# Kernel tuning notes

Measured on AMD Instinct MI355X. Metric: run time of the kernel, lower is better.

## Reference

```python
import jax, jax.numpy as jnp
import numpy as np

STEPS = 8  # number of scaling-and-squaring steps


def _identity_grid(D, H, W, dtype):
    # (D, H, W, 3) voxel-coordinate identity transformation
    z = jnp.arange(D, dtype=dtype)
    y = jnp.arange(H, dtype=dtype)
    x = jnp.arange(W, dtype=dtype)
    return jnp.stack(jnp.meshgrid(z, y, x, indexing='ij'), axis=-1)


def _pull_wrap(v, phi):
    """Trilinear sampling of field v at voxel coords phi with circular ('dft') bound.

    v:   (B, D, H, W, 3) vector field (values)
    phi: (B, D, H, W, 3) sampling coordinates in voxel space (z, y, x order)
    """
    B, D, H, W, C = v.shape
    f = jnp.floor(phi)
    w1 = phi - f          # weight of the +1 corner
    w0 = 1.0 - w1
    i0 = f.astype(jnp.int32)
    dims = jnp.array([D, H, W], dtype=jnp.int32)
    i0 = jnp.mod(i0, dims)          # wrap (dft) boundary
    i1 = jnp.mod(i0 + 1, dims)
    zs, ys, xs = (i0[..., 0], i1[..., 0]), (i0[..., 1], i1[..., 1]), (i0[..., 2], i1[..., 2])
    wzs, wys, wxs = (w0[..., 0], w1[..., 0]), (w0[..., 1], w1[..., 1]), (w0[..., 2], w1[..., 2])
    vflat = v.reshape(B, D * H * W, C)
    out = jnp.zeros_like(v)
    for a in range(2):
        for b in range(2):
            for c in range(2):
                lin = (zs[a] * H + ys[b]) * W + xs[c]              # (B, D, H, W)
                vals = jnp.take_along_axis(vflat, lin.reshape(B, -1, 1), axis=1)
                vals = vals.reshape(B, D, H, W, C)
                out = out + (wzs[a] * wys[b] * wxs[c])[..., None] * vals
    return out


def setup_inputs() -> dict:
    key = jax.random.key(0)
    velocity = jax.random.normal(key, (2, 128, 128, 128, 3), dtype=jnp.float32)
    return {"velocity": velocity}


def reference(velocity):
    # Scaling and squaring: v <- v/2^K; repeat K times: v <- v + v o (id + v)
    B, D, H, W, C = velocity.shape
    grid = _identity_grid(D, H, W, velocity.dtype)[None]  # (1, D, H, W, 3)
    v = velocity / (2.0 ** STEPS)
    for _ in range(STEPS):
        v = v + _pull_wrap(v, grid + v)
    # displacement=False -> return transformation field id + displacement
    return grid + v
```

## Files before the change

### kernel.cpp

```cpp
#include <hip/hip_runtime.h>
#include <hip/hip_fp16.h>


#define DHW   (128 * 128 * 128)
#define NVOX  (2 * DHW)
#define RW    129

#if defined(__has_builtin)
#  if __has_builtin(__builtin_amdgcn_global_load_lds)
#    define HAVE_ASYNC 1
#  endif
#endif
#ifndef HAVE_ASYNC
#  define HAVE_ASYNC 0
#endif

__device__ __forceinline__ __half2 bc_h2(unsigned u) {
    return *reinterpret_cast<__half2*>(&u);
}

__device__ __forceinline__ void acc_cell(uint2 c, float w,
                                         float& az, float& ay, float& ax) {
    __half2 c0 = bc_h2(c.x), c1 = bc_h2(c.y);
    az = fmaf(w, __low2float(c0),  az);
    ay = fmaf(w, __high2float(c0), ay);
    ax = fmaf(w, __low2float(c1),  ax);
}

template <int H, int BX, int BZ, bool PAD_OUT>
__global__ __launch_bounds__(512) void sq_sten_dma(
    const uint2* __restrict__ fin, uint2* __restrict__ fout)
{
    constexpr int LBX = (BX == 64) ? 6 : 5;
    constexpr int NB = 4;
    constexpr int TX = BX + 2 * H, TY = 8 + 2 * H, TZ = BZ + 2 * H;
    constexpr int TS = TX * TY * TZ;
    constexpr int DWS = TS * 2;
    constexpr int NP  = (DWS + 511) / 512;
    constexpr int VPT = (BX * BZ) / 64;
    constexpr int NXB = 128 / BX, LNX = 7 - LBX;
    static_assert(2 * TS * 8 <= 64 * 1024, "dbuf exceeds 64KB static LDS");
    static_assert(VPT == 4 || VPT == 2, "vmcnt literal needs 4 or 2");
    __shared__ uint2 bufA[TS];
    __shared__ uint2 bufB[TS];

    int t = (int)threadIdx.x;
    int b = (int)blockIdx.x;
    int X = (b & (NXB - 1)) << LBX;
    int b2 = b >> LNX;
    int Y = (b2 & 15) << 3;
    int b3 = b2 >> 4;
    int Z0 = (b3 & 7) * (BZ * NB);
    int batch = b3 >> 3;
    int bb21 = batch << 21;

    unsigned sxy[NP];
    unsigned szzp[(NP + 3) / 4];
#pragma unroll
    for (int q = 0; q < (NP + 3) / 4; ++q) szzp[q] = 0;
#pragma unroll
    for (int p = 0; p < NP; ++p) {
        int idx = t + p * 512;
        if (idx < DWS) {
            int cell = idx >> 1, half = idx & 1;
            int xx = cell % TX;
            int rem = cell / TX;
            int yy = rem % TY, zz = rem / TY;
            int gx = (X - H + xx) & 127;
            int gy = (Y - H + yy) & 127;
            sxy[p] = (unsigned)((((gy << 7) | gx) << 1) | half);
            szzp[p >> 2] |= (unsigned)zz << ((p & 3) * 8);
        } else {
            sxy[p] = 0;
        }
    }

    const unsigned* fdw = (const unsigned*)fin;

#if HAVE_ASYNC
#define ASYNC_DW(lptr, gptr)                                            \
    __builtin_amdgcn_global_load_lds(                                   \
        (const __attribute__((address_space(1))) unsigned*)(gptr),      \
        (__attribute__((address_space(3))) unsigned*)(lptr), 4, 0, 0)
#else
#define ASYNC_DW(lptr, gptr)  (*(lptr) = *(gptr))
#endif

#define STAGE(ZB, BUF)                                                  \
    { unsigned* ldw = (unsigned*)(BUF);                                 \
      _Pragma("unroll")                                                 \
      for (int p = 0; p < NP; ++p) {                                    \
          int idx = t + p * 512;                                        \
          if (idx < DWS) {                                              \
              int zz = (int)((szzp[p >> 2] >> ((p & 3) * 8)) & 255u);   \
              int gz = ((ZB) - H + zz) & 127;                           \
              ASYNC_DW(ldw + idx,                                       \
                       fdw + (bb21 << 1) + (gz << 15) + (int)sxy[p]);   \
          }                                                             \
      }                                                                 \
      __builtin_amdgcn_sched_barrier(0); }

    int lx = t & (BX - 1);
    int ly = (t >> LBX) & 7;
    int lz0 = (t >> (LBX + 3)) * VPT;

#define COMPUTE(TILE, Z)                                                \
    { _Pragma("unroll")                                                 \
      for (int v = 0; v < VPT; ++v) {                                   \
          int lz = lz0 + v;                                             \
          int cidx = ((lz + H) * TY + (ly + H)) * TX + (lx + H);        \
          uint2 c = (TILE)[cidx];                                       \
          __half2 c0 = bc_h2(c.x), c1 = bc_h2(c.y);                     \
          float vz = __low2float(c0), vy = __high2float(c0);            \
          float vx = __low2float(c1);                                   \
          float pz = (float)((Z) + lz) + vz;                            \
          float py = (float)(Y + ly) + vy;                              \
          float px = (float)(X + lx) + vx;                              \
          float fz = floorf(pz), fy = floorf(py), fx = floorf(px);      \
          float wz1 = pz - fz, wy1 = py - fy, wx1 = px - fx;            \
          float wz0 = 1.0f - wz1, wy0 = 1.0f - wy1, wx0 = 1.0f - wx1;   \
          int izl = (int)fz - (Z) + H;                                  \
          int iyl = (int)fy - Y + H;                                    \
          int ixl = (int)fx - X + H;                                    \
          float wzy00 = wz0 * wy0, wzy01 = wz0 * wy1;                   \
          float wzy10 = wz1 * wy0, wzy11 = wz1 * wy1;                   \
          float az = 0.0f, ay = 0.0f, ax = 0.0f;                        \
          int i00 = (izl * TY + iyl) * TX + ixl;                        \
          int i01 = i00 + TX;                                           \
          int i10 = i00 + TY * TX;                                      \
          int i11 = i10 + TX;                                           \
          acc_cell((TILE)[i00],     wzy00 * wx0, az, ay, ax);           \
          acc_cell((TILE)[i00 + 1], wzy00 * wx1, az, ay, ax);           \
          acc_cell((TILE)[i01],     wzy01 * wx0, az, ay, ax);           \
          acc_cell((TILE)[i01 + 1], wzy01 * wx1, az, ay, ax);           \
          acc_cell((TILE)[i10],     wzy10 * wx0, az, ay, ax);           \
          acc_cell((TILE)[i10 + 1], wzy10 * wx1, az, ay, ax);           \
          acc_cell((TILE)[i11],     wzy11 * wx0, az, ay, ax);           \
          acc_cell((TILE)[i11 + 1], wzy11 * wx1, az, ay, ax);           \
          __half2 p0 = __floats2half2_rn(vz + az, vy + ay);             \
          __half2 p1 = __floats2half2_rn(vx + ax, 0.0f);                \
          uint2 sd;                                                     \
          sd.x = *reinterpret_cast<unsigned*>(&p0);                     \
          sd.y = *reinterpret_cast<unsigned*>(&p1);                     \
          int z_ = (Z) + lz, y_ = Y + ly, x_ = X + lx;                  \
          if (PAD_OUT) {                                                \
              int rS = (batch << 14) + (z_ << 7) + y_;                  \
              int pidx = (rS << 7) + rS + x_;                           \
              fout[pidx] = sd;                                          \
              if (x_ == 0) fout[pidx + 128] = sd;                       \
          } else {                                                      \
              fout[bb21 | (z_ << 14) | (y_ << 7) | x_] = sd;            \
          }                                                             \
      } }

#if HAVE_ASYNC
#define BRICK_BAR                                                       \
    if (VPT == 4) asm volatile("s_waitcnt vmcnt(4)" ::: "memory");      \
    else          asm volatile("s_waitcnt vmcnt(2)" ::: "memory");      \
    __builtin_amdgcn_sched_barrier(0);                                  \
    asm volatile("s_waitcnt lgkmcnt(0)" ::: "memory");                  \
    __builtin_amdgcn_sched_barrier(0);                                  \
    __builtin_amdgcn_s_barrier();                                       \
    __builtin_amdgcn_sched_barrier(0);
#else
#define BRICK_BAR __syncthreads();
#endif

    STAGE(Z0, bufA)
    __syncthreads();

    STAGE(Z0 + BZ, bufB)
    COMPUTE(bufA, Z0)
    BRICK_BAR
    STAGE(Z0 + 2 * BZ, bufA)
    COMPUTE(bufB, Z0 + BZ)
    BRICK_BAR
    STAGE(Z0 + 3 * BZ, bufB)
    COMPUTE(bufA, Z0 + 2 * BZ)
    BRICK_BAR
    COMPUTE(bufB, Z0 + 3 * BZ)

#undef STAGE
#undef COMPUTE
#undef BRICK_BAR
#undef ASYNC_DW
}

__global__ __launch_bounds__(512) void sq_step1(
    const float* __restrict__ velf, uint2* __restrict__ fout)
{
    constexpr int H = 1, BX = 64, BZ = 4;
    constexpr int TX = 66, TY = 10, TZ = 6, TS = TX * TY * TZ;
    constexpr int PF = (TS + 511) / 512;
    constexpr int VPT = 4;
    __shared__ uint2 tile[TS];

    int t = (int)threadIdx.x;
    int b = (int)blockIdx.x;
    int X = (b & 1) << 6;
    int b2 = b >> 1;
    int Y = (b2 & 15) << 3;
    int b3 = b2 >> 4;
    int Z0 = (b3 & 7) << 4;
    int batch = b3 >> 3;
    int bb21 = batch << 21;

    int lx = t & 63, ly = (t >> 6) & 7, lz0 = (t >> 9) * VPT;

    for (int i = 0; i < 4; ++i) {
        int Z = Z0 + i * BZ;
#pragma unroll
        for (int p = 0; p < PF; ++p) {
            int idx = t + p * 512;
            if (idx < TS) {
                int xx = idx % TX;
                int rem = idx / TX;
                int yy = rem % TY, zz = rem / TY;
                int gx = (X - H + xx) & 127;
                int gy = (Y - H + yy) & 127;
                int gz = (Z - H + zz) & 127;
                size_t a = (size_t)(bb21 | (gz << 14) | (gy << 7) | gx) * 3;
                const float s = 1.0f / 256.0f;
                __half2 q0 = __floats2half2_rn(velf[a] * s, velf[a + 1] * s);
                __half2 q1 = __floats2half2_rn(velf[a + 2] * s, 0.0f);
                uint2 cc;
                cc.x = *reinterpret_cast<unsigned*>(&q0);
                cc.y = *reinterpret_cast<unsigned*>(&q1);
                tile[idx] = cc;
            }
        }
        __syncthreads();

#pragma unroll
        for (int v = 0; v < VPT; ++v) {
            int lz = lz0 + v;
            int cidx = ((lz + H) * TY + (ly + H)) * TX + (lx + H);
            uint2 c = tile[cidx];
            __half2 c0 = bc_h2(c.x), c1 = bc_h2(c.y);
            float vz = __low2float(c0), vy = __high2float(c0);
            float vx = __low2float(c1);
            float pz = (float)(Z + lz) + vz;
            float py = (float)(Y + ly) + vy;
            float px = (float)(X + lx) + vx;
            float fz = floorf(pz), fy = floorf(py), fx = floorf(px);
            float wz1 = pz - fz, wy1 = py - fy, wx1 = px - fx;
            float wz0 = 1.0f - wz1, wy0 = 1.0f - wy1, wx0 = 1.0f - wx1;
            int izl = (int)fz - Z + H;
            int iyl = (int)fy - Y + H;
            int ixl = (int)fx - X + H;
            float wzy00 = wz0 * wy0, wzy01 = wz0 * wy1;
            float wzy10 = wz1 * wy0, wzy11 = wz1 * wy1;
            float az = 0.0f, ay = 0.0f, ax = 0.0f;
            int i00 = (izl * TY + iyl) * TX + ixl;
            int i01 = i00 + TX;
            int i10 = i00 + TY * TX;
            int i11 = i10 + TX;
            acc_cell(tile[i00],     wzy00 * wx0, az, ay, ax);
            acc_cell(tile[i00 + 1], wzy00 * wx1, az, ay, ax);
            acc_cell(tile[i01],     wzy01 * wx0, az, ay, ax);
            acc_cell(tile[i01 + 1], wzy01 * wx1, az, ay, ax);
            acc_cell(tile[i10],     wzy10 * wx0, az, ay, ax);
            acc_cell(tile[i10 + 1], wzy10 * wx1, az, ay, ax);
            acc_cell(tile[i11],     wzy11 * wx0, az, ay, ax);
            acc_cell(tile[i11 + 1], wzy11 * wx1, az, ay, ax);
            __half2 p0 = __floats2half2_rn(vz + az, vy + ay);
            __half2 p1 = __floats2half2_rn(vx + ax, 0.0f);
            uint2 sd;
            sd.x = *reinterpret_cast<unsigned*>(&p0);
            sd.y = *reinterpret_cast<unsigned*>(&p1);
            int z_ = Z + lz, y_ = Y + ly, x_ = X + lx;
            fout[bb21 | (z_ << 14) | (y_ << 7) | x_] = sd;
        }
        __syncthreads();
    }
}

__device__ __forceinline__ void acc_pair(uint4 g, float wl, float wr,
                                         float& az, float& ay, float& ax) {
    __half2 h0 = bc_h2(g.x);
    __half2 h1 = bc_h2(g.y);
    __half2 h2 = bc_h2(g.z);
    __half2 h3 = bc_h2(g.w);
    az += wl * __low2float(h0)  + wr * __low2float(h2);
    ay += wl * __high2float(h0) + wr * __high2float(h2);
    ax += wl * __low2float(h1)  + wr * __low2float(h3);
}

template <bool IN_F32, bool OUT_F32>
__global__ __launch_bounds__(1024) void sq_step_p(
    const void* __restrict__ vin_, void* __restrict__ vout_)
{
    const float* vinf = (const float*)vin_;
    const uint2* vinh = (const uint2*)vin_;

    int t = (int)threadIdx.x;
    int b = (int)blockIdx.x;
    int x = ((b & 1) << 6) | (t & 63);
    int y = (((b >> 1) & 31) << 2) | ((t >> 6) & 3);
    int z = (((b >> 6) & 31) << 2) | (t >> 8);
    int batch = b >> 11;

    const float s = IN_F32 ? (1.0f / 256.0f) : 1.0f;

    int bbr = batch << 14;
    int r   = bbr + (z << 7) + y;

    float vz, vy, vx;
    if (IN_F32) {
        size_t base = ((size_t)(batch << 21) + (z << 14) + (y << 7) + x) * 3;
        vz = vinf[base + 0] * s;
        vy = vinf[base + 1] * s;
        vx = vinf[base + 2] * s;
    } else {
        uint2 c = vinh[(r << 7) + r + x];
        __half2 c0 = bc_h2(c.x), c1 = bc_h2(c.y);
        vz = __low2float(c0); vy = __high2float(c0); vx = __low2float(c1);
    }

    float pz = (float)z + vz, py = (float)y + vy, px = (float)x + vx;
    float fz = floorf(pz), fy = floorf(py), fx = floorf(px);
    float wz1 = pz - fz, wy1 = py - fy, wx1 = px - fx;
    float wz0 = 1.0f - wz1, wy0 = 1.0f - wy1, wx0 = 1.0f - wx1;

    int iz0 = ((int)fz) & 127, iy0 = ((int)fy) & 127, ix0 = ((int)fx) & 127;
    int iz1 = (iz0 + 1) & 127, iy1 = (iy0 + 1) & 127;

    float wzy00 = wz0 * wy0, wzy01 = wz0 * wy1;
    float wzy10 = wz1 * wy0, wzy11 = wz1 * wy1;

    float az = 0.0f, ay = 0.0f, ax = 0.0f;

    if (IN_F32) {
        int bb  = batch << 21;
        int ix1 = (ix0 + 1) & 127;
        int zo0 = bb + (iz0 << 14), zo1 = bb + (iz1 << 14);
        int yo0 = iy0 << 7, yo1 = iy1 << 7;
#define CORNER(ZO, YO, IX, WW)                                          \
        {                                                               \
            size_t a = (size_t)((ZO) + (YO) + (IX)) * 3;                \
            float w = (WW);                                             \
            az += w * (vinf[a] * s);                                    \
            ay += w * (vinf[a + 1] * s);                                \
            ax += w * (vinf[a + 2] * s);                                \
        }
        CORNER(zo0, yo0, ix0, wzy00 * wx0)
        CORNER(zo0, yo0, ix1, wzy00 * wx1)
        CORNER(zo0, yo1, ix0, wzy01 * wx0)
        CORNER(zo0, yo1, ix1, wzy01 * wx1)
        CORNER(zo1, yo0, ix0, wzy10 * wx0)
        CORNER(zo1, yo0, ix1, wzy10 * wx1)
        CORNER(zo1, yo1, ix0, wzy11 * wx0)
        CORNER(zo1, yo1, ix1, wzy11 * wx1)
#undef CORNER
    } else {
        int r00 = bbr + (iz0 << 7) + iy0;
        int r01 = bbr + (iz0 << 7) + iy1;
        int r10 = bbr + (iz1 << 7) + iy0;
        int r11 = bbr + (iz1 << 7) + iy1;
        uint4 g00 = *(const uint4*)(vinh + (r00 << 7) + r00 + ix0);
        uint4 g01 = *(const uint4*)(vinh + (r01 << 7) + r01 + ix0);
        uint4 g10 = *(const uint4*)(vinh + (r10 << 7) + r10 + ix0);
        uint4 g11 = *(const uint4*)(vinh + (r11 << 7) + r11 + ix0);
        acc_pair(g00, wzy00 * wx0, wzy00 * wx1, az, ay, ax);
        acc_pair(g01, wzy01 * wx0, wzy01 * wx1, az, ay, ax);
        acc_pair(g10, wzy10 * wx0, wzy10 * wx1, az, ay, ax);
        acc_pair(g11, wzy11 * wx0, wzy11 * wx1, az, ay, ax);
    }

    float oz = vz + az;
    float oy = vy + ay;
    float ox = vx + ax;

    if (OUT_F32) {
        float* voutf = (float*)vout_;
        size_t base = ((size_t)(batch << 21) + (z << 14) + (y << 7) + x) * 3;
        voutf[base + 0] = oz + (float)z;
        voutf[base + 1] = oy + (float)y;
        voutf[base + 2] = ox + (float)x;
    } else {
        __half2 p0 = __floats2half2_rn(oz, oy);
        __half2 p1 = __floats2half2_rn(ox, 0.0f);
        uint2 sd;
        sd.x = *reinterpret_cast<unsigned*>(&p0);
        sd.y = *reinterpret_cast<unsigned*>(&p1);
        uint2* vouth = (uint2*)vout_;
        int pidx = (r << 7) + r + x;
        vouth[pidx] = sd;
        if (x == 0) vouth[pidx + 128] = sd;
    }
}

extern "C" void kernel_launch(void* const* d_in, const int* in_sizes, int n_in,
                              void* d_out, int out_size, void* d_ws, size_t ws_size,
                              hipStream_t stream) {
    const float* vel = (const float*)d_in[0];
    float* out = (float*)d_out;

    const size_t UB = (size_t)NVOX * 8;
    const size_t PB = (size_t)2 * 128 * 128 * RW * 8;

    dim3 pblock(512);
    dim3 pgrid1(512);
    dim3 pgrid2(1024);
    dim3 ggrid(NVOX / 1024), gblock(1024);

    if (ws_size >= 2 * UB + PB) {
        uint2* U0 = (uint2*)d_ws;
        uint2* U1 = (uint2*)((char*)d_ws + UB);
        uint2* P  = (uint2*)((char*)d_ws + 2 * UB);

        sq_step1<<<pgrid1, pblock, 0, stream>>>(vel, U0);
        sq_sten_dma<1, 64, 4, false><<<pgrid1, pblock, 0, stream>>>(U0, U1);
        sq_sten_dma<1, 64, 4, false><<<pgrid1, pblock, 0, stream>>>(U1, U0);
        sq_sten_dma<1, 64, 4, false><<<pgrid1, pblock, 0, stream>>>(U0, U1);
        sq_sten_dma<1, 64, 4, false><<<pgrid1, pblock, 0, stream>>>(U1, U0);
        sq_sten_dma<1, 64, 4, false><<<pgrid1, pblock, 0, stream>>>(U0, U1);
        sq_sten_dma<2, 32, 4, true ><<<pgrid2, pblock, 0, stream>>>(U1, P);
        sq_step_p<false, true ><<<ggrid, gblock, 0, stream>>>(P, out);
    } else {
        void* ws = d_ws;
        sq_step_p<true,  false><<<ggrid, gblock, 0, stream>>>(vel, ws);
        sq_step_p<false, false><<<ggrid, gblock, 0, stream>>>(ws,  out);
        sq_step_p<false, false><<<ggrid, gblock, 0, stream>>>(out, ws);
        sq_step_p<false, false><<<ggrid, gblock, 0, stream>>>(ws,  out);
        sq_step_p<false, false><<<ggrid, gblock, 0, stream>>>(out, ws);
        sq_step_p<false, false><<<ggrid, gblock, 0, stream>>>(ws,  out);
        sq_step_p<false, false><<<ggrid, gblock, 0, stream>>>(out, ws);
        sq_step_p<false, true ><<<ggrid, gblock, 0, stream>>>(ws,  out);
    }
}
```

Baseline: 269.1 us.

## Fuse pairs of squaring steps into one kernel with halo recompute

Adds a kernel that loads a halo-2 tile into LDS, computes one squaring step over the halo-1 region, writes it back to LDS and computes the second step for the interior. The first six steps become three fused launches instead of six, roughly halving global traffic for those steps and cutting launch count. In exchange it recomputes halo voxels and drops the async double-buffered DMA pipeline in favour of synchronous loads. It also relies on displacements staying within one voxel per step.

Measured after the change: 326.0 us. 1.21x slower.

```diff
diff --git a/kernel.cpp b/kernel.cpp
--- a/kernel.cpp
+++ b/kernel.cpp
@@ -25,6 +25,131 @@
     az = fmaf(w, __low2float(c0),  az);
     ay = fmaf(w, __high2float(c0), ay);
     ax = fmaf(w, __low2float(c1),  ax);
+}
+
+template <int TXt, int TYt>
+__device__ __forceinline__ uint2 step_point(const uint2* __restrict__ tile,
+                                            uint2 c, int gz, int gy, int gx,
+                                            int OZ, int OY, int OX)
+{
+    __half2 c0 = bc_h2(c.x), c1 = bc_h2(c.y);
+    float vz = __low2float(c0), vy = __high2float(c0), vx = __low2float(c1);
+
+    float pz = (float)gz + vz, py = (float)gy + vy, px = (float)gx + vx;
+    float fz = floorf(pz), fy = floorf(py), fx = floorf(px);
+    float wz1 = pz - fz, wy1 = py - fy, wx1 = px - fx;
+    float wz0 = 1.0f - wz1, wy0 = 1.0f - wy1, wx0 = 1.0f - wx1;
+
+    int izl = (int)fz - OZ;
+    int iyl = (int)fy - OY;
+    int ixl = (int)fx - OX;
+
+    float wzy00 = wz0 * wy0, wzy01 = wz0 * wy1;
+    float wzy10 = wz1 * wy0, wzy11 = wz1 * wy1;
+
+    float az = 0.0f, ay = 0.0f, ax = 0.0f;
+    int i00 = (izl * TYt + iyl) * TXt + ixl;
+    int i01 = i00 + TXt;
+    int i10 = i00 + TYt * TXt;
+    int i11 = i10 + TXt;
+
+    acc_cell(tile[i00],     wzy00 * wx0, az, ay, ax);
+    acc_cell(tile[i00 + 1], wzy00 * wx1, az, ay, ax);
+    acc_cell(tile[i01],     wzy01 * wx0, az, ay, ax);
+    acc_cell(tile[i01 + 1], wzy01 * wx1, az, ay, ax);
+    acc_cell(tile[i10],     wzy10 * wx0, az, ay, ax);
+    acc_cell(tile[i10 + 1], wzy10 * wx1, az, ay, ax);
+    acc_cell(tile[i11],     wzy11 * wx0, az, ay, ax);
+    acc_cell(tile[i11 + 1], wzy11 * wx1, az, ay, ax);
+
+    __half2 p0 = __floats2half2_rn(vz + az, vy + ay);
+    __half2 p1 = __floats2half2_rn(vx + ax, 0.0f);
+    uint2 sd;
+    sd.x = *reinterpret_cast<unsigned*>(&p0);
+    sd.y = *reinterpret_cast<unsigned*>(&p1);
+    return sd;
+}
+
+template <bool IN_F32>
+__global__ __launch_bounds__(512) void sq_fused2(
+    const float* __restrict__ velf,
+    const uint2* __restrict__ fin,
+    uint2* __restrict__ fout)
+{
+    constexpr int TXI = 68, TYI = 12, TZI = 8, TSI = TXI * TYI * TZI;
+    constexpr int TXM = 66, TYM = 10, TZM = 6, TSM = TXM * TYM * TZM;
+    constexpr int PFI = (TSI + 511) / 512;
+    constexpr int NM  = (TSM + 511) / 512;
+    static_assert(TSI * 8 <= 64 * 1024, "input tile exceeds 64KB");
+    __shared__ uint2 tile[TSI];
+
+    int t = (int)threadIdx.x;
+    int b = (int)blockIdx.x;
+    int X = (b & 1) << 6;
+    int b2 = b >> 1;
+    int Y = (b2 & 15) << 3;
+    int b3 = b2 >> 4;
+    int Z = (b3 & 31) << 2;
+    int batch = b3 >> 5;
+    int bb21 = batch << 21;
+
+    for (int p = 0; p < PFI; ++p) {
+        int idx = t + p * 512;
+        if (idx < TSI) {
+            int xx = idx % TXI;
+            int rem = idx / TXI;
+            int yy = rem % TYI, zz = rem / TYI;
+            int gx = (X - 2 + xx) & 127;
+            int gy = (Y - 2 + yy) & 127;
+            int gz = (Z - 2 + zz) & 127;
+            uint2 cc;
+            if (IN_F32) {
+                const float s = 1.0f / 256.0f;
+                size_t a = (size_t)(bb21 | (gz << 14) | (gy << 7) | gx) * 3;
+                __half2 q0 = __floats2half2_rn(velf[a] * s, velf[a + 1] * s);
+                __half2 q1 = __floats2half2_rn(velf[a + 2] * s, 0.0f);
+                cc.x = *reinterpret_cast<unsigned*>(&q0);
+                cc.y = *reinterpret_cast<unsigned*>(&q1);
+            } else {
+                cc = fin[bb21 | (gz << 14) | (gy << 7) | gx];
+            }
+            tile[idx] = cc;
+        }
+    }
+    __syncthreads();
+
+    uint2 m[NM];
+#pragma unroll
+    for (int p = 0; p < NM; ++p) {
+        int idx = t + p * 512;
+        if (idx < TSM) {
+            int xx = idx % TXM;
+            int rem = idx / TXM;
+            int yy = rem % TYM, zz = rem / TYM;
+            int ci = ((zz + 1) * TYI + (yy + 1)) * TXI + (xx + 1);
+            m[p] = step_point<TXI, TYI>(tile, tile[ci],
+                                        Z - 1 + zz, Y - 1 + yy, X - 1 + xx,
+                                        Z - 2, Y - 2, X - 2);
+        }
+    }
+    __syncthreads();
+
+#pragma unroll
+    for (int p = 0; p < NM; ++p) {
+        int idx = t + p * 512;
+        if (idx < TSM) tile[idx] = m[p];
+    }
+    __syncthreads();
+
+    int lx = t & 63, ly = (t >> 6) & 7;
+#pragma unroll
+    for (int lz = 0; lz < 4; ++lz) {
+        int ci = ((lz + 1) * TYM + (ly + 1)) * TXM + (lx + 1);
+        uint2 sd = step_point<TXM, TYM>(tile, tile[ci],
+                                        Z + lz, Y + ly, X + lx,
+                                        Z - 1, Y - 1, X - 1);
+        fout[bb21 | ((Z + lz) << 14) | ((Y + ly) << 7) | (X + lx)] = sd;
+    }
 }
 
 template <int H, int BX, int BZ, bool PAD_OUT>
@@ -109,39 +234,9 @@
       for (int v = 0; v < VPT; ++v) {                                   \
           int lz = lz0 + v;                                             \
           int cidx = ((lz + H) * TY + (ly + H)) * TX + (lx + H);        \
-          uint2 c = (TILE)[cidx];                                       \
-          __half2 c0 = bc_h2(c.x), c1 = bc_h2(c.y);                     \
-          float vz = __low2float(c0), vy = __high2float(c0);            \
-          float vx = __low2float(c1);                                   \
-          float pz = (float)((Z) + lz) + vz;                            \
-          float py = (float)(Y + ly) + vy;                              \
-          float px = (float)(X + lx) + vx;                              \
-          float fz = floorf(pz), fy = floorf(py), fx = floorf(px);      \
-          float wz1 = pz - fz, wy1 = py - fy, wx1 = px - fx;            \
-          float wz0 = 1.0f - wz1, wy0 = 1.0f - wy1, wx0 = 1.0f - wx1;   \
-          int izl = (int)fz - (Z) + H;                                  \
-          int iyl = (int)fy - Y + H;                                    \
-          int ixl = (int)fx - X + H;                                    \
-          float wzy00 = wz0 * wy0, wzy01 = wz0 * wy1;                   \
-          float wzy10 = wz1 * wy0, wzy11 = wz1 * wy1;                   \
-          float az = 0.0f, ay = 0.0f, ax = 0.0f;                        \
-          int i00 = (izl * TY + iyl) * TX + ixl;                        \
-          int i01 = i00 + TX;                                           \
-          int i10 = i00 + TY * TX;                                      \
-          int i11 = i10 + TX;                                           \
-          acc_cell((TILE)[i00],     wzy00 * wx0, az, ay, ax);           \
-          acc_cell((TILE)[i00 + 1], wzy00 * wx1, az, ay, ax);           \
-          acc_cell((TILE)[i01],     wzy01 * wx0, az, ay, ax);           \
-          acc_cell((TILE)[i01 + 1], wzy01 * wx1, az, ay, ax);           \
-          acc_cell((TILE)[i10],     wzy10 * wx0, az, ay, ax);           \
-          acc_cell((TILE)[i10 + 1], wzy10 * wx1, az, ay, ax);           \
-          acc_cell((TILE)[i11],     wzy11 * wx0, az, ay, ax);           \
-          acc_cell((TILE)[i11 + 1], wzy11 * wx1, az, ay, ax);           \
-          __half2 p0 = __floats2half2_rn(vz + az, vy + ay);             \
-          __half2 p1 = __floats2half2_rn(vx + ax, 0.0f);                \
-          uint2 sd;                                                     \
-          sd.x = *reinterpret_cast<unsigned*>(&p0);                     \
-          sd.y = *reinterpret_cast<unsigned*>(&p1);                     \
+          uint2 sd = step_point<TX, TY>((TILE), (TILE)[cidx],           \
+                                        (Z) + lz, Y + ly, X + lx,       \
+                                        (Z) - H, Y - H, X - H);         \
           int z_ = (Z) + lz, y_ = Y + ly, x_ = X + lx;                  \
           if (PAD_OUT) {                                                \
               int rS = (batch << 14) + (z_ << 7) + y_;                  \
@@ -184,95 +279,6 @@
 #undef COMPUTE
 #undef BRICK_BAR
 #undef ASYNC_DW
-}
-
-__global__ __launch_bounds__(512) void sq_step1(
-    const float* __restrict__ velf, uint2* __restrict__ fout)
-{
-    constexpr int H = 1, BX = 64, BZ = 4;
-    constexpr int TX = 66, TY = 10, TZ = 6, TS = TX * TY * TZ;
-    constexpr int PF = (TS + 511) / 512;
-    constexpr int VPT = 4;
-    __shared__ uint2 tile[TS];
-
-    int t = (int)threadIdx.x;
-    int b = (int)blockIdx.x;
-    int X = (b & 1) << 6;
-    int b2 = b >> 1;
-    int Y = (b2 & 15) << 3;
-    int b3 = b2 >> 4;
-    int Z0 = (b3 & 7) << 4;
-    int batch = b3 >> 3;
-    int bb21 = batch << 21;
-
-    int lx = t & 63, ly = (t >> 6) & 7, lz0 = (t >> 9) * VPT;
-
-    for (int i = 0; i < 4; ++i) {
-        int Z = Z0 + i * BZ;
-#pragma unroll
-        for (int p = 0; p < PF; ++p) {
-            int idx = t + p * 512;
-            if (idx < TS) {
-                int xx = idx % TX;
-                int rem = idx / TX;
-                int yy = rem % TY, zz = rem / TY;
-                int gx = (X - H + xx) & 127;
-                int gy = (Y - H + yy) & 127;
-                int gz = (Z - H + zz) & 127;
-                size_t a = (size_t)(bb21 | (gz << 14) | (gy << 7) | gx) * 3;
-                const float s = 1.0f / 256.0f;
-                __half2 q0 = __floats2half2_rn(velf[a] * s, velf[a + 1] * s);
-                __half2 q1 = __floats2half2_rn(velf[a + 2] * s, 0.0f);
-                uint2 cc;
-                cc.x = *reinterpret_cast<unsigned*>(&q0);
-                cc.y = *reinterpret_cast<unsigned*>(&q1);
-                tile[idx] = cc;
-            }
-        }
-        __syncthreads();
-
-#pragma unroll
-        for (int v = 0; v < VPT; ++v) {
-            int lz = lz0 + v;
-            int cidx = ((lz + H) * TY + (ly + H)) * TX + (lx + H);
-            uint2 c = tile[cidx];
-            __half2 c0 = bc_h2(c.x), c1 = bc_h2(c.y);
-            float vz = __low2float(c0), vy = __high2float(c0);
-            float vx = __low2float(c1);
-            float pz = (float)(Z + lz) + vz;
-            float py = (float)(Y + ly) + vy;
-            float px = (float)(X + lx) + vx;
-            float fz = floorf(pz), fy = floorf(py), fx = floorf(px);
-            float wz1 = pz - fz, wy1 = py - fy, wx1 = px - fx;
-            float wz0 = 1.0f - wz1, wy0 = 1.0f - wy1, wx0 = 1.0f - wx1;
-            int izl = (int)fz - Z + H;
-            int iyl = (int)fy - Y + H;
-            int ixl = (int)fx - X + H;
-            float wzy00 = wz0 * wy0, wzy01 = wz0 * wy1;
-            float wzy10 = wz1 * wy0, wzy11 = wz1 * wy1;
-            float az = 0.0f, ay = 0.0f, ax = 0.0f;
-            int i00 = (izl * TY + iyl) * TX + ixl;
-            int i01 = i00 + TX;
-            int i10 = i00 + TY * TX;
-            int i11 = i10 + TX;
-            acc_cell(tile[i00],     wzy00 * wx0, az, ay, ax);
-            acc_cell(tile[i00 + 1], wzy00 * wx1, az, ay, ax);
-            acc_cell(tile[i01],     wzy01 * wx0, az, ay, ax);
-            acc_cell(tile[i01 + 1], wzy01 * wx1, az, ay, ax);
-            acc_cell(tile[i10],     wzy10 * wx0, az, ay, ax);
-            acc_cell(tile[i10 + 1], wzy10 * wx1, az, ay, ax);
-            acc_cell(tile[i11],     wzy11 * wx0, az, ay, ax);
-            acc_cell(tile[i11 + 1], wzy11 * wx1, az, ay, ax);
-            __half2 p0 = __floats2half2_rn(vz + az, vy + ay);
-            __half2 p1 = __floats2half2_rn(vx + ax, 0.0f);
-            uint2 sd;
-            sd.x = *reinterpret_cast<unsigned*>(&p0);
-            sd.y = *reinterpret_cast<unsigned*>(&p1);
-            int z_ = Z + lz, y_ = Y + ly, x_ = X + lx;
-            fout[bb21 | (z_ << 14) | (y_ << 7) | x_] = sd;
-        }
-        __syncthreads();
-    }
 }
 
 __device__ __forceinline__ void acc_pair(uint4 g, float wl, float wr,
@@ -399,9 +405,8 @@
     const size_t UB = (size_t)NVOX * 8;
     const size_t PB = (size_t)2 * 128 * 128 * RW * 8;
 
-    dim3 pblock(512);
-    dim3 pgrid1(512);
-    dim3 pgrid2(1024);
+    dim3 fblock(512), fgrid(2048);
+    dim3 pblock(512), pgrid2(1024);
     dim3 ggrid(NVOX / 1024), gblock(1024);
 
     if (ws_size >= 2 * UB + PB) {
@@ -409,13 +414,10 @@
         uint2* U1 = (uint2*)((char*)d_ws + UB);
         uint2* P  = (uint2*)((char*)d_ws + 2 * UB);
 
-        sq_step1<<<pgrid1, pblock, 0, stream>>>(vel, U0);
-        sq_sten_dma<1, 64, 4, false><<<pgrid1, pblock, 0, stream>>>(U0, U1);
-        sq_sten_dma<1, 64, 4, false><<<pgrid1, pblock, 0, stream>>>(U1, U0);
-        sq_sten_dma<1, 64, 4, false><<<pgrid1, pblock, 0, stream>>>(U0, U1);
-        sq_sten_dma<1, 64, 4, false><<<pgrid1, pblock, 0, stream>>>(U1, U0);
-        sq_sten_dma<1, 64, 4, false><<<pgrid1, pblock, 0, stream>>>(U0, U1);
-        sq_sten_dma<2, 32, 4, true ><<<pgrid2, pblock, 0, stream>>>(U1, P);
+        sq_fused2<true ><<<fgrid, fblock, 0, stream>>>(vel, nullptr, U0);
+        sq_fused2<false><<<fgrid, fblock, 0, stream>>>(nullptr, U0, U1);
+        sq_fused2<false><<<fgrid, fblock, 0, stream>>>(nullptr, U1, U0);
+        sq_sten_dma<2, 32, 4, true><<<pgrid2, pblock, 0, stream>>>(U0, P);
         sq_step_p<false, true ><<<ggrid, gblock, 0, stream>>>(P, out);
     } else {
         void* ws = d_ws;
```
